# Kernel tuning notes

Measured on AMD Instinct MI355X. Metric: run time of the kernel, lower is better.

## Reference

```python
import jax, jax.numpy as jnp
import numpy as np

B, C, H, W = 64, 512, 28, 28
NL = 4  # number of (layer, attention) pairs iterated over


def setup_inputs() -> dict:
    key = jax.random.key(0)
    ks = jax.random.split(key, 6)
    n = lambda k, sh: jax.random.normal(k, sh, dtype=jnp.float32) * 0.05
    return {
        "x": n(ks[0], (B, C, H, W)),
        "w_ih_l1": n(ks[1], (C // 16, C)),
        "b_ih_l1": jnp.zeros((C // 16,), jnp.float32),
        "w_ih_l2": n(ks[2], (3 * C, C // 16)),
        "b_ih_l2": jnp.zeros((3 * C,), jnp.float32),
        "w_hh_l1": n(ks[3], (C // 16, C)),
        "b_hh_l1": jnp.zeros((C // 16,), jnp.float32),
        "w_hh_l2": n(ks[4], (3 * C, C // 16)),
        "b_hh_l2": jnp.zeros((3 * C,), jnp.float32),
        "dw_kernel": n(ks[5], (C, 1, 3, 3)),  # depthwise 3x3, groups=C, no bias
        "num_layers": NL,
    }


def reference(x, w_ih_l1, b_ih_l1, w_ih_l2, b_ih_l2,
              w_hh_l1, b_hh_l1, w_hh_l2, b_hh_l2, dw_kernel, num_layers):
    # DSU cell (nlayers=1): bottleneck MLP gates, LSTM-style state update.
    def cell(inp, hx, cx):
        g_i = jnp.dot(jax.nn.relu(jnp.dot(inp, w_ih_l1.T) + b_ih_l1), w_ih_l2.T) + b_ih_l2
        g_h = jnp.dot(jax.nn.relu(jnp.dot(hx, w_hh_l1.T) + b_hh_l1), w_hh_l2.T) + b_hh_l2
        i_g, f_g, c_g = jnp.split(g_i + g_h, 3, axis=-1)
        ncx = jax.nn.sigmoid(f_g) * cx + jax.nn.sigmoid(i_g) * jnp.tanh(c_g)
        return jax.nn.sigmoid(ncx), ncx

    b, c = x.shape[0], x.shape[1]
    ht = jnp.zeros((b, c), x.dtype)
    ct = jnp.zeros((b, c), x.dtype)

    for _ in range(int(num_layers)):
        org = x  # layer stub: layer(x) -> (x, x)
        # recurrent SE path on pooled features
        seq = jnp.mean(x, axis=(2, 3))  # [B, C]
        ht, ct = cell(seq, ht, ct)
        # second DSU call: original indexes hidden[0][0] on a [B,C] tensor,
        # i.e. uses batch element 0 as hx/cx (broadcast) -- replicated faithfully.
        y_in = jnp.mean(org, axis=(2, 3))
        out_h, _ = cell(y_in, ht[0], ct[0])  # [B, C]
        # depthwise 3x3 conv on org
        re = jax.lax.conv_general_dilated(
            org, dw_kernel, window_strides=(1, 1), padding="SAME",
            feature_group_count=c, dimension_numbers=("NCHW", "OIHW", "NCHW"))
        org = org * out_h[:, :, None, None] + re
        x = x + org  # attention stub: attention(x, org) -> x + org
    return x
```

## Files before the change

kernel.cpp:

```cpp
#include <hip/hip_runtime.h>


#define HW 784
#define F4 196
#define CC 512
#define BB 64
#define NP 32768
#define TS 31

__device__ __forceinline__ float sigm(float x) { return 1.f / (1.f + __expf(-x)); }

#define STENCIL(src, py, px4, w0,w1,w2,w3,w4,w5,w6,w7,w8, y0,y1,y2,y3) do { \
    const float* r0 = &(src)[(py) * TS + (px4) * 4]; \
    const float* r1 = r0 + TS; \
    const float* r2 = r0 + 2 * TS; \
    float a0=r0[0],a1=r0[1],a2=r0[2],a3=r0[3],a4=r0[4],a5=r0[5]; \
    float b0=r1[0],b1=r1[1],b2=r1[2],b3=r1[3],b4=r1[4],b5=r1[5]; \
    float c0=r2[0],c1=r2[1],c2=r2[2],c3=r2[3],c4=r2[4],c5=r2[5]; \
    y0 = a0*w0+a1*w1+a2*w2 + b0*w3+b1*w4+b2*w5 + c0*w6+c1*w7+c2*w8; \
    y1 = a1*w0+a2*w1+a3*w2 + b1*w3+b2*w4+b3*w5 + c1*w6+c2*w7+c3*w8; \
    y2 = a2*w0+a3*w1+a4*w2 + b2*w3+b3*w4+b4*w5 + c2*w6+c3*w7+c4*w8; \
    y3 = a3*w0+a4*w1+a5*w2 + b3*w3+b4*w4+b5*w5 + c3*w6+c4*w7+c5*w8; \
} while (0)

#define ZERO_HALO(tile) do { \
    if (t < 30) (tile)[t] = 0.f; \
    else if (t < 60) (tile)[29 * TS + (t - 30)] = 0.f; \
    else if (t < 88) (tile)[(t - 59) * TS] = 0.f; \
    else if (t < 116) (tile)[(t - 87) * TS + 29] = 0.f; \
} while (0)

__global__ void __launch_bounds__(256) wj_kernel(const float* __restrict__ dwk,
                                                 float* __restrict__ W) {
    __shared__ float tA[30 * TS], tB[30 * TS];
    __shared__ float s_w[9];
    int c = blockIdx.x, t = threadIdx.x;
    ZERO_HALO(tA); ZERO_HALO(tB);
    if (t < 9) s_w[t] = dwk[c * 9 + 8 - t];
    int py = t / 7, px4 = t - py * 7;
    if (t < F4) {
        float* d = &tA[(py + 1) * TS + px4 * 4 + 1];
        d[0] = d[1] = d[2] = d[3] = 1.f;
    }
    __syncthreads();
    float w0=s_w[0],w1=s_w[1],w2=s_w[2],w3=s_w[3],w4=s_w[4],w5=s_w[5],w6=s_w[6],w7=s_w[7],w8=s_w[8];
    float* src = tA; float* dst = tB;
    for (int it = 1; it <= 3; ++it) {
        if (t < F4) {
            float y0, y1, y2, y3;
            STENCIL(src, py, px4, w0,w1,w2,w3,w4,w5,w6,w7,w8, y0,y1,y2,y3);
            float* d = &dst[(py + 1) * TS + px4 * 4 + 1];
            d[0]=y0; d[1]=y1; d[2]=y2; d[3]=y3;
            ((float4*)(W + ((size_t)(it - 1) * CC + c) * HW))[t] = make_float4(y0,y1,y2,y3);
        }
        __syncthreads();
        float* tmp = src; src = dst; dst = tmp;
    }
}

__global__ void __launch_bounds__(256) stats_kernel(const float* __restrict__ x,
                                                    const float* __restrict__ W,
                                                    float* __restrict__ mu) {
    int wave = threadIdx.x >> 6, lane = threadIdx.x & 63;
    int p = blockIdx.x * 4 + wave;
    int c = p & 511;
    const float4* xv = (const float4*)(x + (size_t)p * HW);
    const float4* w1 = (const float4*)(W + (size_t)c * HW);
    const float4* w2 = (const float4*)(W + ((size_t)CC + c) * HW);
    const float4* w3 = (const float4*)(W + ((size_t)2 * CC + c) * HW);
    float s0 = 0.f, s1 = 0.f, s2 = 0.f, s3 = 0.f;
    for (int j = lane; j < F4; j += 64) {
        float4 v = xv[j], a = w1[j], b = w2[j], d = w3[j];
        s0 += v.x + v.y + v.z + v.w;
        s1 += v.x*a.x + v.y*a.y + v.z*a.z + v.w*a.w;
        s2 += v.x*b.x + v.y*b.y + v.z*b.z + v.w*b.w;
        s3 += v.x*d.x + v.y*d.y + v.z*d.z + v.w*d.w;
    }
    #pragma unroll
    for (int off = 32; off > 0; off >>= 1) {
        s0 += __shfl_down(s0, off, 64);
        s1 += __shfl_down(s1, off, 64);
        s2 += __shfl_down(s2, off, 64);
        s3 += __shfl_down(s3, off, 64);
    }
    if (lane == 0) {
        mu[p]          = s0 * (1.f / 784.f);
        mu[NP + p]     = s1 * (1.f / 784.f);
        mu[2 * NP + p] = s2 * (1.f / 784.f);
        mu[3 * NP + p] = s3 * (1.f / 784.f);
    }
}

__global__ void __launch_bounds__(512) cell_kernel(
        const float* __restrict__ mu, float* __restrict__ coef,
        const float* __restrict__ w_ih1, const float* __restrict__ b_ih1,
        const float* __restrict__ w_ih2, const float* __restrict__ b_ih2,
        const float* __restrict__ w_hh1, const float* __restrict__ b_hh1,
        const float* __restrict__ w_hh2, const float* __restrict__ b_hh2,
        float* __restrict__ G_i, float* __restrict__ ct,
        float* __restrict__ g_hpre, float* __restrict__ g_h2c,
        float* __restrict__ ct0c, int k) {
    __shared__ __align__(16) float s_in[CC];
    __shared__ float s_hid[32];
    __shared__ float s_hid2[32];
    __shared__ float s_g[1536];
    const int b = blockIdx.x, t = threadIdx.x;
    const int p = b * CC + t;

    float c0, c1, c2, c3;
    if (k == 0) {
        c0 = 1.f; c1 = c2 = c3 = 0.f;
        if (t < 32) s_hid2[t] = fmaxf(b_hh1[t], 0.f);
    } else {
        c0 = coef[p]; c1 = coef[NP + p]; c2 = coef[2 * NP + p]; c3 = coef[3 * NP + p];
        const float* g  = G_i + b * 1536;
        const float* gh = g_h2c + (size_t)(k - 1) * 1536;
        float ig = g[t] + gh[t];
        float fg = g[CC + t] + gh[CC + t];
        float cg = g[2 * CC + t] + gh[2 * CC + t];
        float nc = sigm(fg) * ct0c[(k - 1) * CC + t] + sigm(ig) * tanhf(cg);
        float A = 1.f + sigm(nc);
        c3 = A * c3 + c2; c2 = A * c2 + c1; c1 = A * c1 + c0; c0 = A * c0;
    }
    coef[p] = c0; coef[NP + p] = c1; coef[2 * NP + p] = c2; coef[3 * NP + p] = c3;
    s_in[t] = c0 * mu[p] + c1 * mu[NP + p] + c2 * mu[2 * NP + p] + c3 * mu[3 * NP + p];
    __syncthreads();

    {
        int o = t >> 4, q = t & 15;
        const float4* wv4 = (const float4*)(w_ih1 + o * CC) + q * 8;
        const float4* in4 = (const float4*)s_in + q * 8;
        float acc = 0.f;
        #pragma unroll
        for (int j = 0; j < 8; ++j) {
            float4 w = wv4[j], xv = in4[j];
            acc += xv.x*w.x + xv.y*w.y + xv.z*w.z + xv.w*w.w;
        }
        acc += __shfl_down(acc, 8, 64);
        acc += __shfl_down(acc, 4, 64);
        acc += __shfl_down(acc, 2, 64);
        acc += __shfl_down(acc, 1, 64);
        if (q == 0) s_hid[o] = fmaxf(acc + b_ih1[o], 0.f);
    }
    __syncthreads();

    for (int o = t; o < 1536; o += 512) {
        const float4* wv4 = (const float4*)(w_ih2 + o * 32);
        float acc = 0.f;
        #pragma unroll
        for (int j = 0; j < 8; ++j) {
            float4 w = wv4[j];
            acc += s_hid[4*j]*w.x + s_hid[4*j+1]*w.y + s_hid[4*j+2]*w.z + s_hid[4*j+3]*w.w;
        }
        float gi = acc + b_ih2[o];
        G_i[b * 1536 + o] = gi;
        float gh;
        if (k == 0) {
            const float4* hv4 = (const float4*)(w_hh2 + o * 32);
            float a2 = 0.f;
            #pragma unroll
            for (int j = 0; j < 8; ++j) {
                float4 w = hv4[j];
                a2 += s_hid2[4*j]*w.x + s_hid2[4*j+1]*w.y + s_hid2[4*j+2]*w.z + s_hid2[4*j+3]*w.w;
            }
            gh = a2 + b_hh2[o];
        } else {
            gh = g_hpre[b * 1536 + o];
        }
        s_g[o] = gi + gh;
    }
    __syncthreads();

    {
        float ctold = (k == 0) ? 0.f : ct[p];
        float nc = sigm(s_g[CC + t]) * ctold + sigm(s_g[t]) * tanhf(s_g[2 * CC + t]);
        ct[p] = nc;
        if (b == 0) ct0c[k * CC + t] = nc;
        s_in[t] = sigm(nc);
    }
    __syncthreads();

    {
        int o = t >> 4, q = t & 15;
        const float4* wv4 = (const float4*)(w_hh1 + o * CC) + q * 8;
        const float4* in4 = (const float4*)s_in + q * 8;
        float acc = 0.f;
        #pragma unroll
        for (int j = 0; j < 8; ++j) {
            float4 w = wv4[j], xv = in4[j];
            acc += xv.x*w.x + xv.y*w.y + xv.z*w.z + xv.w*w.w;
        }
        acc += __shfl_down(acc, 8, 64);
        acc += __shfl_down(acc, 4, 64);
        acc += __shfl_down(acc, 2, 64);
        acc += __shfl_down(acc, 1, 64);
        if (q == 0) s_hid[o] = fmaxf(acc + b_hh1[o], 0.f);
    }
    __syncthreads();

    for (int o = t; o < 1536; o += 512) {
        const float4* wv4 = (const float4*)(w_hh2 + o * 32);
        float acc = 0.f;
        #pragma unroll
        for (int j = 0; j < 8; ++j) {
            float4 w = wv4[j];
            acc += s_hid[4*j]*w.x + s_hid[4*j+1]*w.y + s_hid[4*j+2]*w.z + s_hid[4*j+3]*w.w;
        }
        acc += b_hh2[o];
        g_hpre[b * 1536 + o] = acc;
        if (b == 0) g_h2c[(size_t)k * 1536 + o] = acc;
    }
}

__device__ __forceinline__ void rdcol(const float4* C4, int cc, float (&D)[28]) {
    const float4* s4 = C4 + cc * 9;
    #pragma unroll
    for (int j = 0; j < 7; ++j) {
        float4 v = s4[j];
        D[4*j] = v.x; D[4*j+1] = v.y; D[4*j+2] = v.z; D[4*j+3] = v.w;
    }
}
__device__ __forceinline__ void zcol(float (&D)[28]) {
    #pragma unroll
    for (int r = 0; r < 28; ++r) D[r] = 0.f;
}
__device__ __forceinline__ void wrcol(float4* C4, int cc, const float (&S)[28]) {
    #pragma unroll
    for (int j = 0; j < 7; ++j)
        C4[cc * 9 + j] = make_float4(S[4*j], S[4*j+1], S[4*j+2], S[4*j+3]);
}

__global__ void __launch_bounds__(256) mega_kernel(
        const float* __restrict__ x, float* __restrict__ out,
        const float* __restrict__ G_i, const float* __restrict__ g_h2c,
        const float* __restrict__ ct0c, const float* __restrict__ coef,
        const float* __restrict__ dwk) {
    __shared__ float lds[8 * 1008];
    const int t = threadIdx.x;
    const int w = t >> 6, lane = t & 63;
    const int h = lane >> 5, c = lane & 31;
    const int pl = 2 * w + h;
    const int p = blockIdx.x * 8 + pl;
    const int b = p >> 9, ch = p & 511;
    const bool act = (c < 28);

    {
        const float4* xg = (const float4*)(x + (size_t)(blockIdx.x * 8 + 2 * w) * HW);
        float4* L = (float4*)(lds + 2 * w * 1008);
        #pragma unroll
        for (int i0 = 0; i0 < 7; ++i0) {
            int i = i0 * 64 + lane;
            if (i < 392) {
                int q = i / 196, rem = i - q * 196;
                int row = rem / 7, c4 = rem - row * 7;
                L[q * 252 + row * 7 + c4] = xg[i];
            }
        }
    }
    asm volatile("" ::: "memory");

    const float* g  = G_i + b * 1536;
    const float* gh = g_h2c + 3 * 1536;
    float ig = g[ch] + gh[ch];
    float fg = g[CC + ch] + gh[CC + ch];
    float cg = g[2 * CC + ch] + gh[2 * CC + ch];
    float ncv = sigm(fg) * ct0c[3 * CC + ch] + sigm(ig) * tanhf(cg);
    float A = 1.f + sigm(ncv);
    float k0 = coef[p], k1 = coef[NP + p], k2 = coef[2 * NP + p], k3 = coef[3 * NP + p];
    float e4 = k3, e3 = A*k3 + k2, e2 = A*k2 + k1, e1 = A*k1 + k0, e0 = A*k0;
    float w0 = dwk[ch*9+0], w1 = dwk[ch*9+1], w2 = dwk[ch*9+2];
    float w3 = dwk[ch*9+3], w4 = dwk[ch*9+4], w5 = dwk[ch*9+5];
    float w6 = dwk[ch*9+6], w7 = dwk[ch*9+7], w8 = dwk[ch*9+8];

    float* P = lds + pl * 1008;
    float4* C4 = (float4*)lds + pl * 252;

    float xr[28], tt[28], l[28], rr[28];

    if (act) {
        #pragma unroll
        for (int r = 0; r < 28; ++r) xr[r] = P[r * 28 + c];
    }
    asm volatile("" ::: "memory");
    if (act) wrcol(C4, c, xr);
    asm volatile("" ::: "memory");

    if (act) {
        if (c > 0) rdcol(C4, c - 1, l); else zcol(l);
        if (c < 27) rdcol(C4, c + 1, rr); else zcol(rr);
        #pragma unroll
        for (int r = 0; r < 28; ++r) {
            float tm1 = (r > 0) ? xr[r-1] : 0.f, tp1 = (r < 27) ? xr[r+1] : 0.f;
            float lm1 = (r > 0) ? l[r-1]  : 0.f, lp1 = (r < 27) ? l[r+1]  : 0.f;
            float rm1 = (r > 0) ? rr[r-1] : 0.f, rp1 = (r < 27) ? rr[r+1] : 0.f;
            float tap = w0*lm1 + w1*tm1 + w2*rm1 + w3*l[r] + w4*xr[r] + w5*rr[r]
                      + w6*lp1 + w7*tp1 + w8*rp1;
            tt[r] = e3 * xr[r] + e4 * tap;
        }
    }
    asm volatile("" ::: "memory");
    if (act) wrcol(C4, c, tt);
    asm volatile("" ::: "memory");

    #pragma unroll
    for (int it = 2; it <= 4; ++it) {
        float e = (it == 2) ? e2 : (it == 3) ? e1 : e0;
        if (act) {
            if (c > 0) rdcol(C4, c - 1, l); else zcol(l);
            if (c < 27) rdcol(C4, c + 1, rr); else zcol(rr);
            float pm1 = 0.f;
            #pragma unroll
            for (int r = 0; r < 28; ++r) {
                float cur = tt[r];
                float tp1 = (r < 27) ? tt[r+1] : 0.f;
                float lm1 = (r > 0) ? l[r-1]  : 0.f, lp1 = (r < 27) ? l[r+1]  : 0.f;
                float rm1 = (r > 0) ? rr[r-1] : 0.f, rp1 = (r < 27) ? rr[r+1] : 0.f;
                float tap = w0*lm1 + w1*pm1 + w2*rm1 + w3*l[r] + w4*cur + w5*rr[r]
                          + w6*lp1 + w7*tp1 + w8*rp1;
                tt[r] = e * xr[r] + tap;
                pm1 = cur;
            }
        }
        asm volatile("" ::: "memory");
        if (it < 4) {
            if (act) wrcol(C4, c, tt);
            asm volatile("" ::: "memory");
        }
    }

    if (act) {
        #pragma unroll
        for (int r = 0; r < 28; ++r) P[r * 28 + c] = tt[r];
    }
    asm volatile("" ::: "memory");
    {
        float4* og = (float4*)(out + (size_t)(blockIdx.x * 8 + 2 * w) * HW);
        const float4* L = (const float4*)(lds + 2 * w * 1008);
        #pragma unroll
        for (int i0 = 0; i0 < 7; ++i0) {
            int i = i0 * 64 + lane;
            if (i < 392) {
                int q = i / 196, rem = i - q * 196;
                int row = rem / 7, c4 = rem - row * 7;
                og[i] = L[q * 252 + row * 7 + c4];
            }
        }
    }
}

extern "C" void kernel_launch(void* const* d_in, const int* in_sizes, int n_in,
                              void* d_out, int out_size, void* d_ws, size_t ws_size,
                              hipStream_t stream) {
    const float* x_in  = (const float*)d_in[0];
    const float* w_ih1 = (const float*)d_in[1];
    const float* b_ih1 = (const float*)d_in[2];
    const float* w_ih2 = (const float*)d_in[3];
    const float* b_ih2 = (const float*)d_in[4];
    const float* w_hh1 = (const float*)d_in[5];
    const float* b_hh1 = (const float*)d_in[6];
    const float* w_hh2 = (const float*)d_in[7];
    const float* b_hh2 = (const float*)d_in[8];
    const float* dwk   = (const float*)d_in[9];
    float* out = (float*)d_out;
    char* ws = (char*)d_ws;

    float* mu    = (float*)(ws + 0);
    float* coef  = (float*)(ws + 524288);
    float* G_i   = (float*)(ws + 1048576);
    float* ct    = (float*)(ws + 1441792);
    float* g_hpre= (float*)(ws + 1572864);
    float* g_h2c = (float*)(ws + 1966080);
    float* ct0c  = (float*)(ws + 1990656);
    float* Wbuf  = (float*)(ws + 1998848);

    wj_kernel<<<512, 256, 0, stream>>>(dwk, Wbuf);
    stats_kernel<<<8192, 256, 0, stream>>>(x_in, Wbuf, mu);
    for (int k = 0; k < 4; ++k)
        cell_kernel<<<BB, 512, 0, stream>>>(mu, coef, w_ih1, b_ih1, w_ih2, b_ih2,
                                            w_hh1, b_hh1, w_hh2, b_hh2,
                                            G_i, ct, g_hpre, g_h2c, ct0c, k);
    mega_kernel<<<4096, 256, 0, stream>>>(x_in, out, G_i, g_h2c, ct0c, coef, dwk);
}
```

Measured before the change: 337.5 us.

## Fuse stencil-weight precompute into stats and collapse four cell launches into one

The stencil-power weights are now computed in shared memory inside the stats kernel, so the global W buffer and its extra pass go away. Each block covers one channel over half the batch. The four per-step cell launches become one kernel per batch row that keeps recurrent state in registers and shared memory. Each block redundantly recomputes batch element 0's recurrence rather than reading it from another block. The final per-plane coefficients e0..e4 are precomputed there, so mega_kernel only loads them. This trades launch count and global round-trips for redundant per-block cell work and lower stats-kernel parallelism (1024 blocks instead of 8192).

```diff
diff --git a/kernel.cpp b/kernel.cpp
--- a/kernel.cpp
+++ b/kernel.cpp
@@ -30,11 +30,14 @@
     else if (t < 116) (tile)[(t - 87) * TS + 29] = 0.f; \
 } while (0)
 
-__global__ void __launch_bounds__(256) wj_kernel(const float* __restrict__ dwk,
-                                                 float* __restrict__ W) {
+__global__ void __launch_bounds__(256) statsW_kernel(const float* __restrict__ x,
+                                                     const float* __restrict__ dwk,
+                                                     float* __restrict__ mu) {
     __shared__ float tA[30 * TS], tB[30 * TS];
     __shared__ float s_w[9];
-    int c = blockIdx.x, t = threadIdx.x;
+    __shared__ __align__(16) float sW[3][HW];
+    const int c = blockIdx.x >> 1, half = blockIdx.x & 1;
+    const int t = threadIdx.x;
     ZERO_HALO(tA); ZERO_HALO(tB);
     if (t < 9) s_w[t] = dwk[c * 9 + 8 - t];
     int py = t / 7, px4 = t - py * 7;
@@ -43,172 +46,184 @@
         d[0] = d[1] = d[2] = d[3] = 1.f;
     }
     __syncthreads();
-    float w0=s_w[0],w1=s_w[1],w2=s_w[2],w3=s_w[3],w4=s_w[4],w5=s_w[5],w6=s_w[6],w7=s_w[7],w8=s_w[8];
-    float* src = tA; float* dst = tB;
-    for (int it = 1; it <= 3; ++it) {
-        if (t < F4) {
-            float y0, y1, y2, y3;
-            STENCIL(src, py, px4, w0,w1,w2,w3,w4,w5,w6,w7,w8, y0,y1,y2,y3);
-            float* d = &dst[(py + 1) * TS + px4 * 4 + 1];
-            d[0]=y0; d[1]=y1; d[2]=y2; d[3]=y3;
-            ((float4*)(W + ((size_t)(it - 1) * CC + c) * HW))[t] = make_float4(y0,y1,y2,y3);
-        }
-        __syncthreads();
-        float* tmp = src; src = dst; dst = tmp;
-    }
-}
-
-__global__ void __launch_bounds__(256) stats_kernel(const float* __restrict__ x,
-                                                    const float* __restrict__ W,
-                                                    float* __restrict__ mu) {
-    int wave = threadIdx.x >> 6, lane = threadIdx.x & 63;
-    int p = blockIdx.x * 4 + wave;
-    int c = p & 511;
-    const float4* xv = (const float4*)(x + (size_t)p * HW);
-    const float4* w1 = (const float4*)(W + (size_t)c * HW);
-    const float4* w2 = (const float4*)(W + ((size_t)CC + c) * HW);
-    const float4* w3 = (const float4*)(W + ((size_t)2 * CC + c) * HW);
-    float s0 = 0.f, s1 = 0.f, s2 = 0.f, s3 = 0.f;
-    for (int j = lane; j < F4; j += 64) {
-        float4 v = xv[j], a = w1[j], b = w2[j], d = w3[j];
-        s0 += v.x + v.y + v.z + v.w;
-        s1 += v.x*a.x + v.y*a.y + v.z*a.z + v.w*a.w;
-        s2 += v.x*b.x + v.y*b.y + v.z*b.z + v.w*b.w;
-        s3 += v.x*d.x + v.y*d.y + v.z*d.z + v.w*d.w;
-    }
-    #pragma unroll
-    for (int off = 32; off > 0; off >>= 1) {
-        s0 += __shfl_down(s0, off, 64);
-        s1 += __shfl_down(s1, off, 64);
-        s2 += __shfl_down(s2, off, 64);
-        s3 += __shfl_down(s3, off, 64);
-    }
-    if (lane == 0) {
-        mu[p]          = s0 * (1.f / 784.f);
-        mu[NP + p]     = s1 * (1.f / 784.f);
-        mu[2 * NP + p] = s2 * (1.f / 784.f);
-        mu[3 * NP + p] = s3 * (1.f / 784.f);
-    }
-}
-
-__global__ void __launch_bounds__(512) cell_kernel(
-        const float* __restrict__ mu, float* __restrict__ coef,
+    {
+        float w0=s_w[0],w1=s_w[1],w2=s_w[2],w3=s_w[3],w4=s_w[4],w5=s_w[5],w6=s_w[6],w7=s_w[7],w8=s_w[8];
+        float* src = tA; float* dst = tB;
+        for (int it = 1; it <= 3; ++it) {
+            if (t < F4) {
+                float y0, y1, y2, y3;
+                STENCIL(src, py, px4, w0,w1,w2,w3,w4,w5,w6,w7,w8, y0,y1,y2,y3);
+                float* d = &dst[(py + 1) * TS + px4 * 4 + 1];
+                d[0]=y0; d[1]=y1; d[2]=y2; d[3]=y3;
+                ((float4*)sW[it - 1])[t] = make_float4(y0, y1, y2, y3);
+            }
+            __syncthreads();
+            float* tmp = src; src = dst; dst = tmp;
+        }
+    }
+    const int wave = t >> 6, lane = t & 63;
+    for (int r = 0; r < 8; ++r) {
+        int b = half * 32 + r * 4 + wave;
+        const float4* xv = (const float4*)(x + (size_t)(b * CC + c) * HW);
+        float s0 = 0.f, s1 = 0.f, s2 = 0.f, s3 = 0.f;
+        for (int j = lane; j < F4; j += 64) {
+            float4 v = xv[j];
+            float4 a = ((const float4*)sW[0])[j];
+            float4 bb = ((const float4*)sW[1])[j];
+            float4 d = ((const float4*)sW[2])[j];
+            s0 += v.x + v.y + v.z + v.w;
+            s1 += v.x*a.x + v.y*a.y + v.z*a.z + v.w*a.w;
+            s2 += v.x*bb.x + v.y*bb.y + v.z*bb.z + v.w*bb.w;
+            s3 += v.x*d.x + v.y*d.y + v.z*d.z + v.w*d.w;
+        }
+        #pragma unroll
+        for (int off = 32; off > 0; off >>= 1) {
+            s0 += __shfl_down(s0, off, 64);
+            s1 += __shfl_down(s1, off, 64);
+            s2 += __shfl_down(s2, off, 64);
+            s3 += __shfl_down(s3, off, 64);
+        }
+        if (lane == 0) {
+            int p = b * CC + c;
+            mu[p]          = s0 * (1.f / 784.f);
+            mu[NP + p]     = s1 * (1.f / 784.f);
+            mu[2 * NP + p] = s2 * (1.f / 784.f);
+            mu[3 * NP + p] = s3 * (1.f / 784.f);
+        }
+    }
+}
+
+__device__ __forceinline__ float matvec32(const float* __restrict__ Wrow,
+                                          const float* __restrict__ hid) {
+    const float4* wv4 = (const float4*)Wrow;
+    float acc = 0.f;
+    #pragma unroll
+    for (int j = 0; j < 8; ++j) {
+        float4 w = wv4[j];
+        acc += hid[4*j]*w.x + hid[4*j+1]*w.y + hid[4*j+2]*w.z + hid[4*j+3]*w.w;
+    }
+    return acc;
+}
+__device__ __forceinline__ void stageA(const float* __restrict__ W,
+                                       const float* __restrict__ bias,
+                                       const float* __restrict__ in,
+                                       float* __restrict__ hid, int t) {
+    int o = t >> 4, q = t & 15;
+    const float4* wv4 = (const float4*)(W + o * CC) + q * 8;
+    const float4* in4 = (const float4*)in + q * 8;
+    float acc = 0.f;
+    #pragma unroll
+    for (int j = 0; j < 8; ++j) {
+        float4 w = wv4[j], xv = in4[j];
+        acc += xv.x*w.x + xv.y*w.y + xv.z*w.z + xv.w*w.w;
+    }
+    acc += __shfl_down(acc, 8, 64);
+    acc += __shfl_down(acc, 4, 64);
+    acc += __shfl_down(acc, 2, 64);
+    acc += __shfl_down(acc, 1, 64);
+    if (q == 0) hid[o] = fmaxf(acc + bias[o], 0.f);
+}
+
+__global__ void __launch_bounds__(512) cell_all_kernel(
+        const float* __restrict__ mu, float* __restrict__ e,
         const float* __restrict__ w_ih1, const float* __restrict__ b_ih1,
         const float* __restrict__ w_ih2, const float* __restrict__ b_ih2,
         const float* __restrict__ w_hh1, const float* __restrict__ b_hh1,
-        const float* __restrict__ w_hh2, const float* __restrict__ b_hh2,
-        float* __restrict__ G_i, float* __restrict__ ct,
-        float* __restrict__ g_hpre, float* __restrict__ g_h2c,
-        float* __restrict__ ct0c, int k) {
+        const float* __restrict__ w_hh2, const float* __restrict__ b_hh2) {
     __shared__ __align__(16) float s_in[CC];
+    __shared__ __align__(16) float s_h[CC];
     __shared__ float s_hid[32];
-    __shared__ float s_hid2[32];
-    __shared__ float s_g[1536];
+    __shared__ float s_gi[2][1536];
+    __shared__ float s_ghp[2][1536];
+    __shared__ float s_gh2[1536];
     const int b = blockIdx.x, t = threadIdx.x;
-    const int p = b * CC + t;
-
-    float c0, c1, c2, c3;
-    if (k == 0) {
-        c0 = 1.f; c1 = c2 = c3 = 0.f;
-        if (t < 32) s_hid2[t] = fmaxf(b_hh1[t], 0.f);
-    } else {
-        c0 = coef[p]; c1 = coef[NP + p]; c2 = coef[2 * NP + p]; c3 = coef[3 * NP + p];
-        const float* g  = G_i + b * 1536;
-        const float* gh = g_h2c + (size_t)(k - 1) * 1536;
-        float ig = g[t] + gh[t];
-        float fg = g[CC + t] + gh[CC + t];
-        float cg = g[2 * CC + t] + gh[2 * CC + t];
-        float nc = sigm(fg) * ct0c[(k - 1) * CC + t] + sigm(ig) * tanhf(cg);
-        float A = 1.f + sigm(nc);
-        c3 = A * c3 + c2; c2 = A * c2 + c1; c1 = A * c1 + c0; c0 = A * c0;
-    }
-    coef[p] = c0; coef[NP + p] = c1; coef[2 * NP + p] = c2; coef[3 * NP + p] = c3;
-    s_in[t] = c0 * mu[p] + c1 * mu[NP + p] + c2 * mu[2 * NP + p] + c3 * mu[3 * NP + p];
+
+    float mu0[4], mub[4];
+    #pragma unroll
+    for (int j = 0; j < 4; ++j) {
+        mu0[j] = mu[j * NP + t];
+        mub[j] = mu[j * NP + b * CC + t];
+    }
+    float cf0[4] = {1.f, 0.f, 0.f, 0.f};
+    float cfb[4] = {1.f, 0.f, 0.f, 0.f};
+    float ct0 = 0.f, ctb = 0.f;
+
+    if (t < 32) s_hid[t] = fmaxf(b_hh1[t], 0.f);
     __syncthreads();
-
-    {
-        int o = t >> 4, q = t & 15;
-        const float4* wv4 = (const float4*)(w_ih1 + o * CC) + q * 8;
-        const float4* in4 = (const float4*)s_in + q * 8;
-        float acc = 0.f;
-        #pragma unroll
-        for (int j = 0; j < 8; ++j) {
-            float4 w = wv4[j], xv = in4[j];
-            acc += xv.x*w.x + xv.y*w.y + xv.z*w.z + xv.w*w.w;
-        }
-        acc += __shfl_down(acc, 8, 64);
-        acc += __shfl_down(acc, 4, 64);
-        acc += __shfl_down(acc, 2, 64);
-        acc += __shfl_down(acc, 1, 64);
-        if (q == 0) s_hid[o] = fmaxf(acc + b_ih1[o], 0.f);
-    }
-    __syncthreads();
-
     for (int o = t; o < 1536; o += 512) {
-        const float4* wv4 = (const float4*)(w_ih2 + o * 32);
-        float acc = 0.f;
-        #pragma unroll
-        for (int j = 0; j < 8; ++j) {
-            float4 w = wv4[j];
-            acc += s_hid[4*j]*w.x + s_hid[4*j+1]*w.y + s_hid[4*j+2]*w.z + s_hid[4*j+3]*w.w;
-        }
-        float gi = acc + b_ih2[o];
-        G_i[b * 1536 + o] = gi;
-        float gh;
-        if (k == 0) {
-            const float4* hv4 = (const float4*)(w_hh2 + o * 32);
-            float a2 = 0.f;
-            #pragma unroll
-            for (int j = 0; j < 8; ++j) {
-                float4 w = hv4[j];
-                a2 += s_hid2[4*j]*w.x + s_hid2[4*j+1]*w.y + s_hid2[4*j+2]*w.z + s_hid2[4*j+3]*w.w;
-            }
-            gh = a2 + b_hh2[o];
-        } else {
-            gh = g_hpre[b * 1536 + o];
-        }
-        s_g[o] = gi + gh;
-    }
-    __syncthreads();
-
-    {
-        float ctold = (k == 0) ? 0.f : ct[p];
-        float nc = sigm(s_g[CC + t]) * ctold + sigm(s_g[t]) * tanhf(s_g[2 * CC + t]);
-        ct[p] = nc;
-        if (b == 0) ct0c[k * CC + t] = nc;
-        s_in[t] = sigm(nc);
-    }
-    __syncthreads();
-
-    {
-        int o = t >> 4, q = t & 15;
-        const float4* wv4 = (const float4*)(w_hh1 + o * CC) + q * 8;
-        const float4* in4 = (const float4*)s_in + q * 8;
-        float acc = 0.f;
-        #pragma unroll
-        for (int j = 0; j < 8; ++j) {
-            float4 w = wv4[j], xv = in4[j];
-            acc += xv.x*w.x + xv.y*w.y + xv.z*w.z + xv.w*w.w;
-        }
-        acc += __shfl_down(acc, 8, 64);
-        acc += __shfl_down(acc, 4, 64);
-        acc += __shfl_down(acc, 2, 64);
-        acc += __shfl_down(acc, 1, 64);
-        if (q == 0) s_hid[o] = fmaxf(acc + b_hh1[o], 0.f);
-    }
-    __syncthreads();
-
-    for (int o = t; o < 1536; o += 512) {
-        const float4* wv4 = (const float4*)(w_hh2 + o * 32);
-        float acc = 0.f;
-        #pragma unroll
-        for (int j = 0; j < 8; ++j) {
-            float4 w = wv4[j];
-            acc += s_hid[4*j]*w.x + s_hid[4*j+1]*w.y + s_hid[4*j+2]*w.z + s_hid[4*j+3]*w.w;
-        }
-        acc += b_hh2[o];
-        g_hpre[b * 1536 + o] = acc;
-        if (b == 0) g_h2c[(size_t)k * 1536 + o] = acc;
+        float acc = matvec32(w_hh2 + o * 32, s_hid) + b_hh2[o];
+        s_ghp[0][o] = acc;
+        s_ghp[1][o] = acc;
+    }
+
+    for (int k = 0; k < 4; ++k) {
+        __syncthreads();
+        s_in[t] = cf0[0]*mu0[0] + cf0[1]*mu0[1] + cf0[2]*mu0[2] + cf0[3]*mu0[3];
+        __syncthreads();
+        stageA(w_ih1, b_ih1, s_in, s_hid, t);
+        __syncthreads();
+        for (int o = t; o < 1536; o += 512)
+            s_gi[0][o] = matvec32(w_ih2 + o * 32, s_hid) + b_ih2[o];
+        __syncthreads();
+        {
+            float gi = s_gi[0][t]        + s_ghp[0][t];
+            float gf = s_gi[0][CC + t]   + s_ghp[0][CC + t];
+            float gc = s_gi[0][2*CC + t] + s_ghp[0][2*CC + t];
+            float nc = sigm(gf) * ct0 + sigm(gi) * tanhf(gc);
+            ct0 = nc;
+            s_h[t] = sigm(nc);
+        }
+        __syncthreads();
+        stageA(w_hh1, b_hh1, s_h, s_hid, t);
+        __syncthreads();
+        for (int o = t; o < 1536; o += 512)
+            s_gh2[o] = matvec32(w_hh2 + o * 32, s_hid) + b_hh2[o];
+        __syncthreads();
+        s_in[t] = cfb[0]*mub[0] + cfb[1]*mub[1] + cfb[2]*mub[2] + cfb[3]*mub[3];
+        __syncthreads();
+        stageA(w_ih1, b_ih1, s_in, s_hid, t);
+        __syncthreads();
+        for (int o = t; o < 1536; o += 512)
+            s_gi[1][o] = matvec32(w_ih2 + o * 32, s_hid) + b_ih2[o];
+        __syncthreads();
+        {
+            float gi = s_gi[1][t]        + s_ghp[1][t];
+            float gf = s_gi[1][CC + t]   + s_ghp[1][CC + t];
+            float gc = s_gi[1][2*CC + t] + s_ghp[1][2*CC + t];
+            float nc = sigm(gf) * ctb + sigm(gi) * tanhf(gc);
+            ctb = nc;
+            s_h[t] = sigm(nc);
+        }
+        __syncthreads();
+        stageA(w_hh1, b_hh1, s_h, s_hid, t);
+        __syncthreads();
+        for (int o = t; o < 1536; o += 512)
+            s_ghp[1][o] = matvec32(w_hh2 + o * 32, s_hid) + b_hh2[o];
+        {
+            float f0 = s_gi[0][CC + t] + s_gh2[CC + t];
+            float i0 = s_gi[0][t]      + s_gh2[t];
+            float c0g = s_gi[0][2*CC + t] + s_gh2[2*CC + t];
+            float A0 = 1.f + sigm(sigm(f0) * ct0 + sigm(i0) * tanhf(c0g));
+            float fb = s_gi[1][CC + t] + s_gh2[CC + t];
+            float ib = s_gi[1][t]      + s_gh2[t];
+            float cbg = s_gi[1][2*CC + t] + s_gh2[2*CC + t];
+            float Ab = 1.f + sigm(sigm(fb) * ct0 + sigm(ib) * tanhf(cbg));
+            if (k < 3) {
+                cf0[3] = A0*cf0[3] + cf0[2]; cf0[2] = A0*cf0[2] + cf0[1];
+                cf0[1] = A0*cf0[1] + cf0[0]; cf0[0] = A0*cf0[0];
+                cfb[3] = Ab*cfb[3] + cfb[2]; cfb[2] = Ab*cfb[2] + cfb[1];
+                cfb[1] = Ab*cfb[1] + cfb[0]; cfb[0] = Ab*cfb[0];
+            } else {
+                int p = b * CC + t;
+                e[4 * NP + p] = cfb[3];
+                e[3 * NP + p] = Ab*cfb[3] + cfb[2];
+                e[2 * NP + p] = Ab*cfb[2] + cfb[1];
+                e[NP + p]     = Ab*cfb[1] + cfb[0];
+                e[p]          = Ab*cfb[0];
+            }
+        }
+        if (k < 3)
+            for (int o = t; o < 1536; o += 512) s_ghp[0][o] = s_gh2[o];
     }
 }
 
@@ -232,16 +247,14 @@
 
 __global__ void __launch_bounds__(256) mega_kernel(
         const float* __restrict__ x, float* __restrict__ out,
-        const float* __restrict__ G_i, const float* __restrict__ g_h2c,
-        const float* __restrict__ ct0c, const float* __restrict__ coef,
-        const float* __restrict__ dwk) {
+        const float* __restrict__ e, const float* __restrict__ dwk) {
     __shared__ float lds[8 * 1008];
     const int t = threadIdx.x;
     const int w = t >> 6, lane = t & 63;
     const int h = lane >> 5, c = lane & 31;
     const int pl = 2 * w + h;
     const int p = blockIdx.x * 8 + pl;
-    const int b = p >> 9, ch = p & 511;
+    const int ch = p & 511;
     const bool act = (c < 28);
 
     {
@@ -259,15 +272,7 @@
     }
     asm volatile("" ::: "memory");
 
-    const float* g  = G_i + b * 1536;
-    const float* gh = g_h2c + 3 * 1536;
-    float ig = g[ch] + gh[ch];
-    float fg = g[CC + ch] + gh[CC + ch];
-    float cg = g[2 * CC + ch] + gh[2 * CC + ch];
-    float ncv = sigm(fg) * ct0c[3 * CC + ch] + sigm(ig) * tanhf(cg);
-    float A = 1.f + sigm(ncv);
-    float k0 = coef[p], k1 = coef[NP + p], k2 = coef[2 * NP + p], k3 = coef[3 * NP + p];
-    float e4 = k3, e3 = A*k3 + k2, e2 = A*k2 + k1, e1 = A*k1 + k0, e0 = A*k0;
+    float e0 = e[p], e1 = e[NP + p], e2 = e[2 * NP + p], e3 = e[3 * NP + p], e4 = e[4 * NP + p];
     float w0 = dwk[ch*9+0], w1 = dwk[ch*9+1], w2 = dwk[ch*9+2];
     float w3 = dwk[ch*9+3], w4 = dwk[ch*9+4], w5 = dwk[ch*9+5];
     float w6 = dwk[ch*9+6], w7 = dwk[ch*9+7], w8 = dwk[ch*9+8];
@@ -304,7 +309,7 @@
 
     #pragma unroll
     for (int it = 2; it <= 4; ++it) {
-        float e = (it == 2) ? e2 : (it == 3) ? e1 : e0;
+        float ecur = (it == 2) ? e2 : (it == 3) ? e1 : e0;
         if (act) {
             if (c > 0) rdcol(C4, c - 1, l); else zcol(l);
             if (c < 27) rdcol(C4, c + 1, rr); else zcol(rr);
@@ -317,7 +322,7 @@
                 float rm1 = (r > 0) ? rr[r-1] : 0.f, rp1 = (r < 27) ? rr[r+1] : 0.f;
                 float tap = w0*lm1 + w1*pm1 + w2*rm1 + w3*l[r] + w4*cur + w5*rr[r]
                           + w6*lp1 + w7*tp1 + w8*rp1;
-                tt[r] = e * xr[r] + tap;
+                tt[r] = ecur * xr[r] + tap;
                 pm1 = cur;
             }
         }
@@ -364,20 +369,11 @@
     float* out = (float*)d_out;
     char* ws = (char*)d_ws;
 
-    float* mu    = (float*)(ws + 0);
-    float* coef  = (float*)(ws + 524288);
-    float* G_i   = (float*)(ws + 1048576);
-    float* ct    = (float*)(ws + 1441792);
-    float* g_hpre= (float*)(ws + 1572864);
-    float* g_h2c = (float*)(ws + 1966080);
-    float* ct0c  = (float*)(ws + 1990656);
-    float* Wbuf  = (float*)(ws + 1998848);
-
-    wj_kernel<<<512, 256, 0, stream>>>(dwk, Wbuf);
-    stats_kernel<<<8192, 256, 0, stream>>>(x_in, Wbuf, mu);
-    for (int k = 0; k < 4; ++k)
-        cell_kernel<<<BB, 512, 0, stream>>>(mu, coef, w_ih1, b_ih1, w_ih2, b_ih2,
-                                            w_hh1, b_hh1, w_hh2, b_hh2,
-                                            G_i, ct, g_hpre, g_h2c, ct0c, k);
-    mega_kernel<<<4096, 256, 0, stream>>>(x_in, out, G_i, g_h2c, ct0c, coef, dwk);
-}
+    float* mu = (float*)(ws + 0);
+    float* e  = (float*)(ws + 524288);
+
+    statsW_kernel<<<1024, 256, 0, stream>>>(x_in, dwk, mu);
+    cell_all_kernel<<<BB, 512, 0, stream>>>(mu, e, w_ih1, b_ih1, w_ih2, b_ih2,
+                                            w_hh1, b_hh1, w_hh2, b_hh2);
+    mega_kernel<<<4096, 256, 0, stream>>>(x_in, out, e, dwk);
+}
```

Result: slower. 364.7 us (+8.0%).
